# Performance work log

Hardware: AMD Instinct MI355X
Metric: run time of the kernel (lower is better)

## Reference

```python
import jax, jax.numpy as jnp
import numpy as np

N, E = 30000, 480000
NFEAT, NHID, H1 = 512, 256, 4


def setup_inputs() -> dict:
    key = jax.random.key(0)
    ks = jax.random.split(key, 16)
    rn = lambda k, shp, sc: jax.random.normal(k, shp, jnp.float32) * sc
    return {
        'x': rn(ks[0], (N, NFEAT), 1.0),
        'edge_index': jax.random.randint(ks[1], (2, E), 0, N),
        # layer 1: in=512, out=256, heads=4, D=64
        'w_kqv1': rn(ks[2], (NFEAT, 3 * NHID), NFEAT ** -0.5),
        'b_kqv1': jnp.zeros((3 * NHID,), jnp.float32),
        'k_rel1': rn(ks[3], (H1, NHID // H1, NHID // H1), (NHID // H1) ** -0.5),
        'v_rel1': rn(ks[4], (H1, NHID // H1, NHID // H1), (NHID // H1) ** -0.5),
        'p_rel1': jnp.ones((H1,), jnp.float32),
        'w_out1': rn(ks[5], (NHID, NHID), NHID ** -0.5),
        'b_out1': jnp.zeros((NHID,), jnp.float32),
        'skip1': jnp.ones((1,), jnp.float32),
        'bn_gamma': jnp.ones((NHID,), jnp.float32),
        'bn_beta': jnp.zeros((NHID,), jnp.float32),
        # layer 2: in=256, out=256, heads=1, D=256
        'w_kqv2': rn(ks[6], (NHID, 3 * NHID), NHID ** -0.5),
        'b_kqv2': jnp.zeros((3 * NHID,), jnp.float32),
        'k_rel2': rn(ks[7], (1, NHID, NHID), NHID ** -0.5),
        'v_rel2': rn(ks[8], (1, NHID, NHID), NHID ** -0.5),
        'p_rel2': jnp.ones((1,), jnp.float32),
        'w_out2': rn(ks[9], (NHID, NHID), NHID ** -0.5),
        'b_out2': jnp.zeros((NHID,), jnp.float32),
        'skip2': jnp.ones((1,), jnp.float32),
    }


def hgt_conv(x, edge_index, w_kqv, b_kqv, k_rel, v_rel, p_rel, w_out, b_out, skip, heads):
    n = x.shape[0]
    out_ch = w_out.shape[0]
    d = out_ch // heads
    kqv = x @ w_kqv + b_kqv                      # [n, 3*out]
    k, q, v = jnp.split(kqv, 3, axis=1)
    k = k.reshape(n, heads, d)
    q = q.reshape(n, heads, d)
    v = v.reshape(n, heads, d)
    # relation-specific per-head transforms of source K/V (single edge type)
    kp = jnp.einsum('nhd,hde->nhe', k, k_rel)
    vp = jnp.einsum('nhd,hde->nhe', v, v_rel)
    src, dst = edge_index[0], edge_index[1]
    # edge-wise attention logits, scaled + relation prior
    alpha = jnp.einsum('ehd,ehd->eh', q[dst], kp[src]) * p_rel / jnp.sqrt(jnp.float32(d))
    # segment softmax over incoming edges of each dst node
    amax = jax.ops.segment_max(alpha, dst, num_segments=n)   # [n, H]
    ex = jnp.exp(alpha - amax[dst])
    denom = jax.ops.segment_sum(ex, dst, num_segments=n) + 1e-16
    a = ex / denom[dst]                                      # [E, H]
    agg = jax.ops.segment_sum(a[:, :, None] * vp[src], dst, num_segments=n)
    out = jax.nn.gelu(agg.reshape(n, out_ch), approximate=False) @ w_out + b_out
    if x.shape[1] == out_ch:  # skip gate only when dims match (PyG HGTConv)
        s = jax.nn.sigmoid(skip)
        out = s * out + (1.0 - s) * x
    return out


def reference(x, edge_index, w_kqv1, b_kqv1, k_rel1, v_rel1, p_rel1, w_out1, b_out1,
              skip1, bn_gamma, bn_beta, w_kqv2, b_kqv2, k_rel2, v_rel2, p_rel2,
              w_out2, b_out2, skip2):
    h = hgt_conv(x, edge_index, w_kqv1, b_kqv1, k_rel1, v_rel1, p_rel1,
                 w_out1, b_out1, skip1, heads=4)
    # BatchNorm1d (training-mode batch stats) + ReLU; dropout is identity (eval)
    mu = h.mean(axis=0)
    var = h.var(axis=0)
    h = (h - mu) / jnp.sqrt(var + 1e-5) * bn_gamma + bn_beta
    h = jax.nn.relu(h)
    out = hgt_conv(h, edge_index, w_kqv2, b_kqv2, k_rel2, v_rel2, p_rel2,
                   w_out2, b_out2, skip2, heads=1)
    return out
```

## Files before the change

### kernel.cpp

```cpp
#include <hip/hip_runtime.h>
#include <math.h>

#define NN 30000
#define NE 480000

typedef _Float16 f16x8 __attribute__((ext_vector_type(8)));
typedef _Float16 f16x4 __attribute__((ext_vector_type(4)));
typedef _Float16 f16x2 __attribute__((ext_vector_type(2)));
typedef float f32x4 __attribute__((ext_vector_type(4)));

#define GLOAD_LDS16(gp, lp)                                        \
    __builtin_amdgcn_global_load_lds(                              \
        (const __attribute__((address_space(1))) void*)(gp),       \
        (__attribute__((address_space(3))) void*)(lp), 16, 0, 0)

#define PREP_BLOCKS 9962
__global__ __launch_bounds__(256) void prep_kernel(
    const float* __restrict__ x, _Float16* __restrict__ x_h,
    const float* __restrict__ w_kqv1, _Float16* __restrict__ w1h,
    const float* __restrict__ w_kqv2, _Float16* __restrict__ w2h,
    const float* __restrict__ krel, const float* __restrict__ vrel,
    const float* __restrict__ krel2, const float* __restrict__ vrel2,
    _Float16* __restrict__ rt1, _Float16* __restrict__ rt2,
    const float* __restrict__ b_kqv1, float* __restrict__ bf1,
    const float* __restrict__ b_kqv2, float* __restrict__ bf2,
    const float* __restrict__ w_out1, _Float16* __restrict__ wout1T,
    const float* __restrict__ w_out2, _Float16* __restrict__ wout2T,
    int* __restrict__ deg, float* __restrict__ bnstats)
{
    const int bid = blockIdx.x, tid = threadIdx.x;
    if (bid < 7500) {
        long i = (long)bid * 256 + tid;
        float4 a = ((const float4*)x)[2 * i];
        float4 b = ((const float4*)x)[2 * i + 1];
        f16x8 o = {(_Float16)a.x, (_Float16)a.y, (_Float16)a.z, (_Float16)a.w,
                   (_Float16)b.x, (_Float16)b.y, (_Float16)b.z, (_Float16)b.w};
        ((f16x8*)x_h)[i] = o;
    } else if (bid < 7692) {
        long i = (long)(bid - 7500) * 256 + tid;
        float4 a = ((const float4*)w_kqv1)[2 * i];
        float4 b = ((const float4*)w_kqv1)[2 * i + 1];
        f16x8 o = {(_Float16)a.x, (_Float16)a.y, (_Float16)a.z, (_Float16)a.w,
                   (_Float16)b.x, (_Float16)b.y, (_Float16)b.z, (_Float16)b.w};
        ((f16x8*)w1h)[i] = o;
    } else if (bid < 7788) {
        long i = (long)(bid - 7692) * 256 + tid;
        float4 a = ((const float4*)w_kqv2)[2 * i];
        float4 b = ((const float4*)w_kqv2)[2 * i + 1];
        f16x8 o = {(_Float16)a.x, (_Float16)a.y, (_Float16)a.z, (_Float16)a.w,
                   (_Float16)b.x, (_Float16)b.y, (_Float16)b.z, (_Float16)b.w};
        ((f16x8*)w2h)[i] = o;
    } else if (bid < 8556) {
        int m = bid - 7788;
#pragma unroll
        for (int rep = 0; rep < 3; ++rep) {
            int d = tid + rep * 256;
            _Float16 val = (_Float16)0.0f;
            if (m < 256) {
                if (d < 256 && (d >> 6) == (m >> 6))
                    val = (_Float16)krel[(m >> 6) * 4096 + (d & 63) * 64 + (m & 63)];
            } else if (m < 512) {
                if (d == m) val = (_Float16)1.0f;
            } else {
                if (d >= 512 && ((d - 512) >> 6) == ((m - 512) >> 6))
                    val = (_Float16)vrel[((m - 512) >> 6) * 4096 +
                                         ((d - 512) & 63) * 64 + ((m - 512) & 63)];
            }
            rt1[(long)m * 768 + d] = val;
        }
    } else if (bid < 9324) {
        int m = bid - 8556;
#pragma unroll
        for (int rep = 0; rep < 3; ++rep) {
            int d = tid + rep * 256;
            _Float16 val = (_Float16)0.0f;
            if (m < 256) {
                if (d < 256) val = (_Float16)krel2[(long)d * 256 + m];
            } else if (m < 512) {
                if (d == m) val = (_Float16)1.0f;
            } else {
                if (d >= 512) val = (_Float16)vrel2[(long)(d - 512) * 256 + (m - 512)];
            }
            rt2[(long)m * 768 + d] = val;
        }
    } else if (bid < 9327) {
        int n = (bid - 9324) * 256 + tid;
        float acc;
        if (n < 256) {
            int h = n >> 6, e = n & 63;
            acc = 0.f;
            for (int d = 0; d < 64; ++d) acc += b_kqv1[h * 64 + d] * krel[h * 4096 + d * 64 + e];
        } else if (n < 512) {
            acc = b_kqv1[n];
        } else {
            int m2 = n - 512, h = m2 >> 6, e = m2 & 63;
            acc = 0.f;
            for (int d = 0; d < 64; ++d) acc += b_kqv1[512 + h * 64 + d] * vrel[h * 4096 + d * 64 + e];
        }
        bf1[n] = acc;
    } else if (bid < 9330) {
        int n = (bid - 9327) * 256 + tid;
        float acc;
        if (n < 256) {
            acc = 0.f;
            for (int d = 0; d < 256; ++d) acc += b_kqv2[d] * krel2[(long)d * 256 + n];
        } else if (n < 512) {
            acc = b_kqv2[n];
        } else {
            acc = 0.f;
            for (int d = 0; d < 256; ++d) acc += b_kqv2[512 + d] * vrel2[(long)d * 256 + (n - 512)];
        }
        bf2[n] = acc;
    } else if (bid < 9586) {
        int k = bid - 9330;
        int n = tid;
        wout1T[(long)n * 256 + k] = (_Float16)w_out1[(long)k * 256 + n];
    } else if (bid < 9842) {
        int k = bid - 9586;
        int n = tid;
        wout2T[(long)n * 256 + k] = (_Float16)w_out2[(long)k * 256 + n];
    } else if (bid < 9960) {
        int i = (bid - 9842) * 256 + tid;
        if (i < NN) deg[i] = 0;
    } else {
        int i = (bid - 9960) * 256 + tid;
        if (i < 512) bnstats[i] = 0.0f;
    }
}

__global__ void deg_kernel(const int* __restrict__ dst, int* __restrict__ deg, int e) {
    int i = blockIdx.x * blockDim.x + threadIdx.x;
    if (i < e) atomicAdd(&deg[dst[i]], 1);
}

__global__ __launch_bounds__(1024) void scan_kernel(
    const int* __restrict__ deg, int* __restrict__ row_start,
    int* __restrict__ pos, int n)
{
    __shared__ int smem[1024];
    const int t = threadIdx.x;
    const int base = t * 32;
    int loc[32];
    int s = 0;
#pragma unroll
    for (int g = 0; g < 8; ++g) {
        int idx = base + g * 4;
        int4 d4;
        if (idx + 3 < n) {
            d4 = *(const int4*)(deg + idx);
        } else {
            d4.x = (idx + 0 < n) ? deg[idx + 0] : 0;
            d4.y = (idx + 1 < n) ? deg[idx + 1] : 0;
            d4.z = (idx + 2 < n) ? deg[idx + 2] : 0;
            d4.w = (idx + 3 < n) ? deg[idx + 3] : 0;
        }
        loc[g * 4 + 0] = s; s += d4.x;
        loc[g * 4 + 1] = s; s += d4.y;
        loc[g * 4 + 2] = s; s += d4.z;
        loc[g * 4 + 3] = s; s += d4.w;
    }
    smem[t] = s;
    __syncthreads();
    for (int off = 1; off < 1024; off <<= 1) {
        int tv = 0;
        if (t >= off) tv = smem[t - off];
        __syncthreads();
        smem[t] += tv;
        __syncthreads();
    }
    const int excl = smem[t] - s;
#pragma unroll
    for (int g = 0; g < 32; ++g) {
        int idx = base + g;
        if (idx < n) {
            int r = excl + loc[g];
            row_start[idx] = r;
            pos[idx] = r;
        }
    }
    if (t == 1023) row_start[n] = smem[1023];
}

__global__ void fill_kernel(const int* __restrict__ src, const int* __restrict__ dst,
                            int* __restrict__ pos, int* __restrict__ csr_src, int e) {
    int i = blockIdx.x * blockDim.x + threadIdx.x;
    if (i < e) {
        int p = atomicAdd(&pos[dst[i]], 1);
        csr_src[p] = src[i];
    }
}

__global__ __launch_bounds__(256) void mfma_gemm_kernel(
    const _Float16* __restrict__ A, int lda,
    const _Float16* __restrict__ BT,
    float* __restrict__ Cf,
    _Float16* __restrict__ Ch,
    int ldc, int M, int N, int K,
    const float* __restrict__ bias,
    const _Float16* __restrict__ res,
    const float* __restrict__ skip,
    float* __restrict__ bn_accum)
{
    __shared__ __align__(16) _Float16 As[128][32];
    __shared__ __align__(16) _Float16 Bs[128][32];
    const int tid = threadIdx.x;
    const int bm = blockIdx.y * 128, bn = blockIdx.x * 128;
    const int wave = tid >> 6, lane = tid & 63;
    const int wr = wave >> 1, wc = wave & 1;
    const int l16 = lane & 15, quad = lane >> 4;

    const int r0 = tid >> 2, kc0 = (tid & 3) * 8;
    const int r1 = r0 + 64;
    int gra0 = bm + r0; if (gra0 >= M) gra0 = M - 1;
    int gra1 = bm + r1; if (gra1 >= M) gra1 = M - 1;
    const _Float16* a0 = A + (long)gra0 * lda + kc0;
    const _Float16* a1 = A + (long)gra1 * lda + kc0;
    const _Float16* b0 = BT + (long)(bn + r0) * K + kc0;
    const _Float16* b1 = BT + (long)(bn + r1) * K + kc0;

    auto ldsA = (__attribute__((address_space(3))) char*)&As[0][0];
    auto ldsB = (__attribute__((address_space(3))) char*)&Bs[0][0];
    const int wb = wave * 1024;

    f32x4 acc[4][4] = {};

    for (int k0 = 0; k0 < K; k0 += 32) {
        GLOAD_LDS16(a0 + k0, ldsA + wb);
        GLOAD_LDS16(a1 + k0, ldsA + 4096 + wb);
        GLOAD_LDS16(b0 + k0, ldsB + wb);
        GLOAD_LDS16(b1 + k0, ldsB + 4096 + wb);
        __syncthreads();
        f16x8 af[4], bf[4];
#pragma unroll
        for (int i = 0; i < 4; ++i)
            af[i] = *(const f16x8*)&As[64 * wr + 16 * i + l16][quad * 8];
#pragma unroll
        for (int j = 0; j < 4; ++j)
            bf[j] = *(const f16x8*)&Bs[64 * wc + 16 * j + l16][quad * 8];
#pragma unroll
        for (int i = 0; i < 4; ++i)
#pragma unroll
            for (int j = 0; j < 4; ++j)
                acc[i][j] = __builtin_amdgcn_mfma_f32_16x16x32_f16(af[i], bf[j], acc[i][j], 0, 0, 0);
        __syncthreads();
    }

    float s = 1.0f, om = 0.0f;
    if (skip) {
        float sv = 1.0f / (1.0f + __expf(-skip[0]));
        s = sv; om = 1.0f - sv;
    }
    float cs[4] = {}, cq[4] = {};
#pragma unroll
    for (int i = 0; i < 4; ++i) {
        int gr0 = bm + 64 * wr + 16 * i + quad * 4;
#pragma unroll
        for (int j = 0; j < 4; ++j) {
            int gc = bn + 64 * wc + 16 * j + l16;
            float bv = bias ? bias[gc] : 0.0f;
#pragma unroll
            for (int r = 0; r < 4; ++r) {
                int row = gr0 + r;
                if (row >= M) continue;
                float v = acc[i][j][r] + bv;
                if (res) v = s * v + om * (float)res[(long)row * ldc + gc];
                if (Cf) Cf[(long)row * ldc + gc] = v;
                if (Ch) Ch[(long)row * ldc + gc] = (_Float16)v;
                if (bn_accum) { cs[j] += v; cq[j] += v * v; }
            }
        }
    }
    if (bn_accum) {
        float* redS = (float*)&As[0][0];
        float* redQ = (float*)&Bs[0][0];
        int slot = wr * 4 + quad;
#pragma unroll
        for (int j = 0; j < 4; ++j) {
            int cl = 64 * wc + 16 * j + l16;
            redS[cl * 8 + slot] = cs[j];
            redQ[cl * 8 + slot] = cq[j];
        }
        __syncthreads();
        if (tid < 128) {
            float ssum = 0.f, qsum = 0.f;
#pragma unroll
            for (int t = 0; t < 8; ++t) {
                ssum += redS[tid * 8 + t];
                qsum += redQ[tid * 8 + t];
            }
            atomicAdd(&bn_accum[bn + tid], ssum);
            atomicAdd(&bn_accum[256 + bn + tid], qsum);
        }
    }
}

template <int H>
__global__ __launch_bounds__(256) void attn_f16kv_kernel(
    const _Float16* __restrict__ qbase, int ldq,
    const _Float16* __restrict__ kp, const _Float16* __restrict__ vp, int ldkv,
    const float* __restrict__ p_rel,
    const int* __restrict__ row_start, const int* __restrict__ csr_src,
    _Float16* __restrict__ agg, int n)
{
    constexpr int D = 256 / H;
    constexpr int GL = D / 8;
    int node = blockIdx.x * 4 + (threadIdx.x >> 6);
    int lane = threadIdx.x & 63;
    int half = lane >> 5;
    int l32 = lane & 31;
    if (node >= n) return;
    const int head = l32 / GL;
    const float scale = p_rel[head] * rsqrtf((float)D);
    const int ch = l32 * 8;
    f16x8 qv = *(const f16x8*)(qbase + (long)node * ldq + ch);
    f16x2 qp[4];
#pragma unroll
    for (int j = 0; j < 4; ++j) { qp[j][0] = qv[2 * j]; qp[j][1] = qv[2 * j + 1]; }

    const _Float16* kpc = kp + ch;
    const _Float16* vpc = vp + ch;
    int e0all = row_start[node], e1all = row_start[node + 1];
    int c0 = (e1all - e0all + 1) >> 1;
    int e0 = half ? (e0all + c0) : e0all;
    int e1 = half ? e1all : (e0all + c0);

    float m = -1e30f, lsum = 0.0f;
    float a[8] = {};

    int e = e0;
    for (; e + 1 < e1; e += 2) {
        int s0 = csr_src[e], s1 = csr_src[e + 1];
        f16x8 k0 = *(const f16x8*)(kpc + (long)s0 * ldkv);
        f16x8 k1 = *(const f16x8*)(kpc + (long)s1 * ldkv);
        f16x8 v0 = *(const f16x8*)(vpc + (long)s0 * ldkv);
        f16x8 v1 = *(const f16x8*)(vpc + (long)s1 * ldkv);
        float d0 = 0.0f, d1 = 0.0f;
#pragma unroll
        for (int j = 0; j < 4; ++j) {
            f16x2 k0p = {k0[2 * j], k0[2 * j + 1]};
            f16x2 k1p = {k1[2 * j], k1[2 * j + 1]};
            d0 = __builtin_amdgcn_fdot2(qp[j], k0p, d0, false);
            d1 = __builtin_amdgcn_fdot2(qp[j], k1p, d1, false);
        }
#pragma unroll
        for (int off = 1; off < GL; off <<= 1) {
            d0 += __shfl_xor(d0, off);
            d1 += __shfl_xor(d1, off);
        }
        float al0 = d0 * scale, al1 = d1 * scale;
        float mx = fmaxf(al0, al1);
        float diff = mx - m;
        if (__builtin_expect(diff > 8.0f, 0)) {
            float corr = __expf(-diff);
            lsum *= corr;
#pragma unroll
            for (int j = 0; j < 8; ++j) a[j] *= corr;
            m = mx;
        }
        float w0 = __expf(al0 - m), w1 = __expf(al1 - m);
        lsum += w0 + w1;
#pragma unroll
        for (int j = 0; j < 8; ++j)
            a[j] += w0 * (float)v0[j] + w1 * (float)v1[j];
    }
    if (e < e1) {
        int s0 = csr_src[e];
        f16x8 k0 = *(const f16x8*)(kpc + (long)s0 * ldkv);
        f16x8 v0 = *(const f16x8*)(vpc + (long)s0 * ldkv);
        float d0 = 0.0f;
#pragma unroll
        for (int j = 0; j < 4; ++j) {
            f16x2 k0p = {k0[2 * j], k0[2 * j + 1]};
            d0 = __builtin_amdgcn_fdot2(qp[j], k0p, d0, false);
        }
#pragma unroll
        for (int off = 1; off < GL; off <<= 1) d0 += __shfl_xor(d0, off);
        float al0 = d0 * scale;
        float diff = al0 - m;
        if (__builtin_expect(diff > 8.0f, 0)) {
            float corr = __expf(-diff);
            lsum *= corr;
#pragma unroll
            for (int j = 0; j < 8; ++j) a[j] *= corr;
            m = al0;
        }
        float w0 = __expf(al0 - m);
        lsum += w0;
#pragma unroll
        for (int j = 0; j < 8; ++j) a[j] += w0 * (float)v0[j];
    }

    float m_o = __shfl_xor(m, 32);
    float ls_o = __shfl_xor(lsum, 32);
    float mm = fmaxf(m, m_o);
    float wsf = __expf(m - mm), wo = __expf(m_o - mm);
    lsum = lsum * wsf + ls_o * wo;
#pragma unroll
    for (int j = 0; j < 8; ++j) {
        float a_o = __shfl_xor(a[j], 32);
        a[j] = a[j] * wsf + a_o * wo;
    }

    if (half == 0) {
        float inv = 1.0f / (lsum + 1e-16f);
        f16x8 o;
#pragma unroll
        for (int j = 0; j < 8; ++j) {
            float v = a[j] * inv;
            v = 0.5f * v * (1.0f + erff(v * 0.70710678118654752f));
            o[j] = (_Float16)v;
        }
        *(f16x8*)(agg + (long)node * 256 + ch) = o;
    }
}

__global__ void bn_apply_kernel(const _Float16* __restrict__ hin, _Float16* __restrict__ hbn,
                                const float* __restrict__ stats,
                                const float* __restrict__ gamma, const float* __restrict__ beta) {
    long idx = blockIdx.x * (long)blockDim.x + threadIdx.x;
    if (idx >= (long)NN * 32) return;
    int cg = (int)(idx & 31) * 8;
    f16x8 hv = ((const f16x8*)hin)[idx];
    const float invn = 1.0f / 30000.0f;
    f16x8 o;
#pragma unroll
    for (int r = 0; r < 8; ++r) {
        int c = cg + r;
        float mu = stats[c] * invn;
        float var = stats[256 + c] * invn - mu * mu;
        float v = ((float)hv[r] - mu) * rsqrtf(var + 1e-5f) * gamma[c] + beta[c];
        o[r] = (_Float16)fmaxf(v, 0.0f);
    }
    ((f16x8*)hbn)[idx] = o;
}

extern "C" void kernel_launch(void* const* d_in, const int* in_sizes, int n_in,
                              void* d_out, int out_size, void* d_ws, size_t ws_size,
                              hipStream_t stream) {
    const float* x       = (const float*)d_in[0];
    const int*   ei      = (const int*)d_in[1];
    const float* w_kqv1  = (const float*)d_in[2];
    const float* b_kqv1  = (const float*)d_in[3];
    const float* k_rel1  = (const float*)d_in[4];
    const float* v_rel1  = (const float*)d_in[5];
    const float* p_rel1  = (const float*)d_in[6];
    const float* w_out1  = (const float*)d_in[7];
    const float* b_out1  = (const float*)d_in[8];
    const float* bn_gamma = (const float*)d_in[10];
    const float* bn_beta  = (const float*)d_in[11];
    const float* w_kqv2  = (const float*)d_in[12];
    const float* b_kqv2  = (const float*)d_in[13];
    const float* k_rel2  = (const float*)d_in[14];
    const float* v_rel2  = (const float*)d_in[15];
    const float* p_rel2  = (const float*)d_in[16];
    const float* w_out2  = (const float*)d_in[17];
    const float* b_out2  = (const float*)d_in[18];
    const float* skip2   = (const float*)d_in[19];
    float* out = (float*)d_out;

    char* p = (char*)d_ws;
    auto alloc = [&](size_t bytes) -> void* {
        void* r = (void*)p;
        p += (bytes + 255) & ~(size_t)255;
        return r;
    };
    _Float16* x_h   = (_Float16*)alloc((size_t)NN * 512 * 2);
    _Float16* kqv_h = (_Float16*)alloc((size_t)NN * 768 * 2);
    _Float16* agg_h = (_Float16*)alloc((size_t)NN * 256 * 2);
    _Float16* h16   = (_Float16*)alloc((size_t)NN * 256 * 2);
    _Float16* hbn_h = (_Float16*)alloc((size_t)NN * 256 * 2);
    _Float16* w1h    = (_Float16*)alloc((size_t)512 * 768 * 2);
    _Float16* w2h    = (_Float16*)alloc((size_t)256 * 768 * 2);
    _Float16* rt1    = (_Float16*)alloc((size_t)768 * 768 * 2);
    _Float16* rt2    = (_Float16*)alloc((size_t)768 * 768 * 2);
    _Float16* w1T    = (_Float16*)alloc((size_t)768 * 512 * 2);
    _Float16* w2T    = (_Float16*)alloc((size_t)768 * 256 * 2);
    _Float16* wout1T = (_Float16*)alloc((size_t)256 * 256 * 2);
    _Float16* wout2T = (_Float16*)alloc((size_t)256 * 256 * 2);
    float* bf1       = (float*)alloc(768 * 4);
    float* bf2       = (float*)alloc(768 * 4);
    int*   deg       = (int*)alloc((size_t)NN * 4);
    int*   row_start = (int*)alloc((size_t)(NN + 1) * 4);
    int*   pos       = (int*)alloc((size_t)NN * 4);
    int*   csr_src   = (int*)alloc((size_t)NE * 4);
    float* bnstats   = (float*)alloc(512 * 4);

    const int* esrc = ei;
    const int* edst = ei + NE;

    prep_kernel<<<PREP_BLOCKS, 256, 0, stream>>>(
        x, x_h, w_kqv1, w1h, w_kqv2, w2h, k_rel1, v_rel1, k_rel2, v_rel2,
        rt1, rt2, b_kqv1, bf1, b_kqv2, bf2, w_out1, wout1T, w_out2, wout2T,
        deg, bnstats);

    mfma_gemm_kernel<<<dim3(4, 6), 256, 0, stream>>>(
        rt1, 768, w1h, nullptr, w1T, 512, 768, 512, 768, nullptr, nullptr, nullptr, nullptr);
    mfma_gemm_kernel<<<dim3(2, 6), 256, 0, stream>>>(
        rt2, 768, w2h, nullptr, w2T, 256, 768, 256, 768, nullptr, nullptr, nullptr, nullptr);

    deg_kernel<<<(NE + 255) / 256, 256, 0, stream>>>(edst, deg, NE);
    scan_kernel<<<1, 1024, 0, stream>>>(deg, row_start, pos, NN);
    fill_kernel<<<(NE + 255) / 256, 256, 0, stream>>>(esrc, edst, pos, csr_src, NE);

    const int MB = (NN + 127) / 128;

    mfma_gemm_kernel<<<dim3(6, MB), 256, 0, stream>>>(
        x_h, 512, w1T, nullptr, kqv_h, 768, NN, 768, 512, bf1, nullptr, nullptr, nullptr);
    attn_f16kv_kernel<4><<<(NN + 3) / 4, 256, 0, stream>>>(
        kqv_h + 256, 768, kqv_h, kqv_h + 512, 768, p_rel1, row_start, csr_src, agg_h, NN);
    mfma_gemm_kernel<<<dim3(2, MB), 256, 0, stream>>>(
        agg_h, 256, wout1T, nullptr, h16, 256, NN, 256, 256, b_out1, nullptr, nullptr, bnstats);

    bn_apply_kernel<<<(NN * 32 + 255) / 256, 256, 0, stream>>>(h16, hbn_h, bnstats, bn_gamma, bn_beta);

    mfma_gemm_kernel<<<dim3(6, MB), 256, 0, stream>>>(
        hbn_h, 256, w2T, nullptr, kqv_h, 768, NN, 768, 256, bf2, nullptr, nullptr, nullptr);
    attn_f16kv_kernel<1><<<(NN + 3) / 4, 256, 0, stream>>>(
        kqv_h + 256, 768, kqv_h, kqv_h + 512, 768, p_rel2, row_start, csr_src, agg_h, NN);
    mfma_gemm_kernel<<<dim3(2, MB), 256, 0, stream>>>(
        agg_h, 256, wout2T, out, nullptr, 256, NN, 256, 256, b_out2, hbn_h, skip2, nullptr);
}
```

Baseline: 593.0 us.

## Double-buffer LDS tiles in MFMA GEMM to overlap global loads with compute

The GEMM kernel now keeps two LDS buffers for the A and B tiles. It prefetches the next K-slice with global_load_lds while the MFMAs run on the current slice, so it needs one barrier per iteration instead of two. The goal is to hide global load latency behind MFMA work. This doubles LDS use per block, which may lower occupancy. It also addresses Bs through a fixed offset from As, which assumes the compiler places the two shared arrays back to back.

```diff
diff --git a/kernel.cpp b/kernel.cpp
--- a/kernel.cpp
+++ b/kernel.cpp
@@ -201,8 +201,8 @@
     const float* __restrict__ skip,
     float* __restrict__ bn_accum)
 {
-    __shared__ __align__(16) _Float16 As[128][32];
-    __shared__ __align__(16) _Float16 Bs[128][32];
+    __shared__ __align__(16) _Float16 As[2][128][32];
+    __shared__ __align__(16) _Float16 Bs[2][128][32];
     const int tid = threadIdx.x;
     const int bm = blockIdx.y * 128, bn = blockIdx.x * 128;
     const int wave = tid >> 6, lane = tid & 63;
@@ -218,31 +218,42 @@
     const _Float16* b0 = BT + (long)(bn + r0) * K + kc0;
     const _Float16* b1 = BT + (long)(bn + r1) * K + kc0;
 
-    auto ldsA = (__attribute__((address_space(3))) char*)&As[0][0];
-    auto ldsB = (__attribute__((address_space(3))) char*)&Bs[0][0];
+    auto lds = (__attribute__((address_space(3))) char*)&As[0][0][0];
     const int wb = wave * 1024;
 
     f32x4 acc[4][4] = {};
-
-    for (int k0 = 0; k0 < K; k0 += 32) {
-        GLOAD_LDS16(a0 + k0, ldsA + wb);
-        GLOAD_LDS16(a1 + k0, ldsA + 4096 + wb);
-        GLOAD_LDS16(b0 + k0, ldsB + wb);
-        GLOAD_LDS16(b1 + k0, ldsB + 4096 + wb);
-        __syncthreads();
+    const int nt = K >> 5;
+
+    GLOAD_LDS16(a0, lds + wb);
+    GLOAD_LDS16(a1, lds + 4096 + wb);
+    GLOAD_LDS16(b0, lds + 16384 + wb);
+    GLOAD_LDS16(b1, lds + 16384 + 4096 + wb);
+    __syncthreads();
+
+    int cur = 0;
+    for (int t = 0; t < nt; ++t) {
+        if (t + 1 < nt) {
+            const int k1 = (t + 1) << 5;
+            const int nb = (cur ^ 1) * 8192;
+            GLOAD_LDS16(a0 + k1, lds + nb + wb);
+            GLOAD_LDS16(a1 + k1, lds + nb + 4096 + wb);
+            GLOAD_LDS16(b0 + k1, lds + 16384 + nb + wb);
+            GLOAD_LDS16(b1 + k1, lds + 16384 + nb + 4096 + wb);
+        }
         f16x8 af[4], bf[4];
 #pragma unroll
         for (int i = 0; i < 4; ++i)
-            af[i] = *(const f16x8*)&As[64 * wr + 16 * i + l16][quad * 8];
+            af[i] = *(const f16x8*)&As[cur][64 * wr + 16 * i + l16][quad * 8];
 #pragma unroll
         for (int j = 0; j < 4; ++j)
-            bf[j] = *(const f16x8*)&Bs[64 * wc + 16 * j + l16][quad * 8];
+            bf[j] = *(const f16x8*)&Bs[cur][64 * wc + 16 * j + l16][quad * 8];
 #pragma unroll
         for (int i = 0; i < 4; ++i)
 #pragma unroll
             for (int j = 0; j < 4; ++j)
                 acc[i][j] = __builtin_amdgcn_mfma_f32_16x16x32_f16(af[i], bf[j], acc[i][j], 0, 0, 0);
         __syncthreads();
+        cur ^= 1;
     }
 
     float s = 1.0f, om = 0.0f;
@@ -271,8 +282,8 @@
         }
     }
     if (bn_accum) {
-        float* redS = (float*)&As[0][0];
-        float* redQ = (float*)&Bs[0][0];
+        float* redS = (float*)&As[0][0][0];
+        float* redQ = (float*)&Bs[0][0][0];
         int slot = wr * 4 + quad;
 #pragma unroll
         for (int j = 0; j < 4; ++j) {
```

New measurement: 589.2 us. No clear change (-0.6%).
